# Performance work log

Measured on AMD Instinct MI355X. Metric: run time of the kernel, lower is better.

Reference implementation:

```python
import jax, jax.numpy as jnp
import numpy as np

B, L, D = 1, 2048, 2048
H, KV, HD = 32, 8, 64
REP = H // KV  # GQA repeat factor = 4


def _rope(t, cos, sin):
    # t: (B, L, nH, HD); cos/sin: (L, HD//2). Complex rotation on (even, odd) pairs.
    tr = t.reshape(*t.shape[:-1], HD // 2, 2)
    xr, xi = tr[..., 0], tr[..., 1]
    c = cos[None, :, None, :]
    s = sin[None, :, None, :]
    out_r = xr * c - xi * s
    out_i = xr * s + xi * c
    return jnp.stack([out_r, out_i], axis=-1).reshape(t.shape)


def setup_inputs() -> dict:
    key = jax.random.key(0)
    ks = jax.random.split(key, 5)
    x = jax.random.normal(ks[0], (B, L, D), jnp.float32)
    wq = jax.random.normal(ks[1], (D, H * HD), jnp.float32) * 0.02
    wk = jax.random.normal(ks[2], (D, KV * HD), jnp.float32) * 0.02
    wv = jax.random.normal(ks[3], (D, KV * HD), jnp.float32) * 0.02
    wo = jax.random.normal(ks[4], (H * HD, D), jnp.float32) * 0.02
    pos = jnp.arange(L, dtype=jnp.float32)
    inv_freq = 1.0 / (10000.0 ** (jnp.arange(0, HD, 2, dtype=jnp.float32) / HD))
    ang = pos[:, None] * inv_freq[None, :]  # (L, HD//2)
    freqs_cos = jnp.cos(ang)
    freqs_sin = jnp.sin(ang)
    # causal additive mask (L, L): 0 on/below diagonal, large negative above
    causal = jnp.arange(L)[None, :] <= jnp.arange(L)[:, None]
    mask = jnp.where(causal, 0.0, -1e9).astype(jnp.float32)
    return {"x": x, "wq": wq, "wk": wk, "wv": wv, "wo": wo,
            "freqs_cos": freqs_cos, "freqs_sin": freqs_sin, "mask": mask}


def reference(x, wq, wk, wv, wo, freqs_cos, freqs_sin, mask):
    q = (x @ wq).reshape(B, L, H, HD)
    k = (x @ wk).reshape(B, L, KV, HD)
    v = (x @ wv).reshape(B, L, KV, HD)
    q = _rope(q, freqs_cos, freqs_sin)
    k = _rope(k, freqs_cos, freqs_sin)
    # GQA: repeat_interleave kv heads
    k = jnp.repeat(k, REP, axis=2)
    v = jnp.repeat(v, REP, axis=2)
    # (B, nH, L, HD)
    q = q.transpose(0, 2, 1, 3)
    k = k.transpose(0, 2, 1, 3)
    v = v.transpose(0, 2, 1, 3)
    scores = jnp.einsum('bhqd,bhkd->bhqk', q, k) / np.float32(np.sqrt(HD))
    scores = scores + mask[None, None, :, :]
    attn = jax.nn.softmax(scores.astype(jnp.float32), axis=-1).astype(q.dtype)
    out = jnp.einsum('bhqk,bhkd->bqhd', attn, v).reshape(B, L, H * HD)
    return out @ wo
```

## Files before the change

### kernel.cpp

```cpp
#include <hip/hip_runtime.h>
#include <hip/hip_bf16.h>

#define L 2048
#define D 2048
#define NH 32
#define NKV 8
#define HD 64

typedef unsigned short u16;
typedef __attribute__((ext_vector_type(8))) short bf16x8;
typedef __attribute__((ext_vector_type(4))) float f32x4;

#define QSCALE 0.1803368801f

#define PANEL_OFF(d0, k) ((((size_t)((d0) >> 7) * 64 + ((k) >> 5)) << 12) + (((d0) & 127) << 5) + ((k) & 31))

__device__ __forceinline__ u16 f2bf(float x) {
    __hip_bfloat16 b = __float2bfloat16(x);
    return *reinterpret_cast<u16*>(&b);
}

__device__ __forceinline__ void gload_lds16(const void* g, void* l) {
    __builtin_amdgcn_global_load_lds(
        (const __attribute__((address_space(1))) unsigned int*)g,
        (__attribute__((address_space(3))) unsigned int*)l, 16, 0, 0);
}

__global__ __launch_bounds__(256) void prep_kernel(
    const float* __restrict__ x, u16* __restrict__ xb,
    const float* __restrict__ wq, const float* __restrict__ wk,
    const float* __restrict__ wv, const float* __restrict__ wo,
    u16* __restrict__ wqkvT, u16* __restrict__ woT)
{
    const int z = blockIdx.z;
    if (z == 4) {
        int i = (blockIdx.y * 64 + blockIdx.x) * 256 + threadIdx.x;
        int e = i * 4;
        int row = e >> 11, k0 = e & 2047;
        float4 v = ((const float4*)x)[i];
        ushort4 o;
        o.x = f2bf(v.x); o.y = f2bf(v.y); o.z = f2bf(v.z); o.w = f2bf(v.w);
        *(ushort4*)&xb[PANEL_OFF(row, k0)] = o;
        return;
    }
    const float* src; u16* dst; int C;
    if (z == 0)      { src = wq; dst = wqkvT;                           C = 2048; }
    else if (z == 1) { src = wk; dst = wqkvT + (size_t)2048 * 2048;     C = 512;  }
    else if (z == 2) { src = wv; dst = wqkvT + (size_t)2560 * 2048;     C = 512;  }
    else             { src = wo; dst = woT;                             C = 2048; }
    const int c0 = blockIdx.x * 32;
    if (c0 >= C) return;
    const int r0 = blockIdx.y * 32;
    __shared__ float tile[32][33];
    const int tx = threadIdx.x & 31, ty = threadIdx.x >> 5;
#pragma unroll
    for (int i = 0; i < 32; i += 8)
        tile[ty + i][tx] = src[(size_t)(r0 + ty + i) * C + c0 + tx];
    __syncthreads();
#pragma unroll
    for (int i = 0; i < 32; i += 8) {
        const int n = c0 + ty + i, k = r0 + tx;
        dst[PANEL_OFF(n, k)] = f2bf(tile[tx][ty + i]);
    }
}

#define VT_LDS 72

template <int MODE>
__global__ __launch_bounds__(256) void gemm4w_kernel(
    const u16* __restrict__ A, const u16* __restrict__ Bt, void* __restrict__ Cout,
    int N, int K, const float* __restrict__ fc, const float* __restrict__ fs,
    u16* __restrict__ vt)
{
    __shared__ __align__(16) u16 As[4][128 * 32];
    __shared__ __align__(16) u16 Bs[4][128 * 32];
    const int tid = threadIdx.x;
    const int w = tid >> 6, lane = tid & 63;

    const int nwg = (int)(gridDim.x * gridDim.y);
    int bid = (int)blockIdx.y * (int)gridDim.x + (int)blockIdx.x;
    bid = (bid & 7) * (nwg >> 3) + (bid >> 3);
    const int m0 = (bid / (int)gridDim.x) * 128, n0 = (bid % (int)gridDim.x) * 128;

    const int l15 = lane & 15, quad = lane >> 4, q8 = quad * 8;
    const int wr = (w >> 1) * 64, wc = (w & 1) * 64;
    const int l8 = lane * 8;
    const int wch = w * 1024;

    const u16* pa = A  + ((size_t)(m0 >> 7) * (K / 32) << 12);
    const u16* pb = Bt + ((size_t)(n0 >> 7) * (K / 32) << 12);

    f32x4 acc[4][4];
#pragma unroll
    for (int i = 0; i < 4; ++i)
#pragma unroll
        for (int j = 0; j < 4; ++j) acc[i][j] = (f32x4){0.f, 0.f, 0.f, 0.f};

    const int nSub = K / 32;
    const int nOut = nSub / 2;
#pragma unroll
    for (int s = 0; s < 4; ++s) {
        const size_t so = (size_t)s << 12;
        gload_lds16(pa + so + wch + l8,       &As[s][wch]);
        gload_lds16(pa + so + wch + 512 + l8, &As[s][wch + 512]);
        gload_lds16(pb + so + wch + l8,       &Bs[s][wch]);
        gload_lds16(pb + so + wch + 512 + l8, &Bs[s][wch + 512]);
    }
    for (int it = 0; it < nOut; ++it) {
        const int s0 = 2 * it, cb0 = s0 & 3, cb1 = (s0 + 1) & 3;
        asm volatile("s_waitcnt vmcnt(8)" ::: "memory");
        asm volatile("s_barrier" ::: "memory");
        bf16x8 a0[4], a1[4], b0[4], b1[4];
#pragma unroll
        for (int t = 0; t < 4; ++t) {
            a0[t] = *(const bf16x8*)&As[cb0][(wr + t * 16 + l15) * 32 + q8];
            b0[t] = *(const bf16x8*)&Bs[cb0][(wc + t * 16 + l15) * 32 + q8];
            a1[t] = *(const bf16x8*)&As[cb1][(wr + t * 16 + l15) * 32 + q8];
            b1[t] = *(const bf16x8*)&Bs[cb1][(wc + t * 16 + l15) * 32 + q8];
        }
        asm volatile("s_waitcnt lgkmcnt(0)" ::: "memory");
        asm volatile("s_barrier" ::: "memory");
        {
            const int sp0 = s0 + 4, sp1 = s0 + 5;
            const size_t k0 = (size_t)((sp0 < nSub) ? sp0 : 0) << 12;
            const size_t k1 = (size_t)((sp1 < nSub) ? sp1 : 0) << 12;
            gload_lds16(pa + k0 + wch + l8,       &As[cb0][wch]);
            gload_lds16(pa + k0 + wch + 512 + l8, &As[cb0][wch + 512]);
            gload_lds16(pb + k0 + wch + l8,       &Bs[cb0][wch]);
            gload_lds16(pb + k0 + wch + 512 + l8, &Bs[cb0][wch + 512]);
            gload_lds16(pa + k1 + wch + l8,       &As[cb1][wch]);
            gload_lds16(pa + k1 + wch + 512 + l8, &As[cb1][wch + 512]);
            gload_lds16(pb + k1 + wch + l8,       &Bs[cb1][wch]);
            gload_lds16(pb + k1 + wch + 512 + l8, &Bs[cb1][wch + 512]);
        }
#pragma unroll
        for (int i = 0; i < 4; ++i)
#pragma unroll
            for (int j = 0; j < 4; ++j) {
                acc[i][j] = __builtin_amdgcn_mfma_f32_16x16x32_bf16(a0[i], b0[j], acc[i][j], 0, 0, 0);
                acc[i][j] = __builtin_amdgcn_mfma_f32_16x16x32_bf16(a1[i], b1[j], acc[i][j], 0, 0, 0);
            }
    }

    if (MODE == 0) {
        float* C = (float*)Cout;
#pragma unroll
        for (int i = 0; i < 4; ++i)
#pragma unroll
            for (int j = 0; j < 4; ++j)
#pragma unroll
                for (int r = 0; r < 4; ++r)
                    C[(size_t)(m0 + wr + i * 16 + quad * 4 + r) * N + n0 + wc + j * 16 + l15] = acc[i][j][r];
    } else {
        __syncthreads();
        u16* O = (u16*)Cout;
        const int vc0 = n0 + wc;
        if (vc0 < 2560) {
            const float scl = (vc0 < 2048) ? QSCALE : 1.0f;
            const int odd = l15 & 1;
#pragma unroll
            for (int i = 0; i < 4; ++i)
#pragma unroll
                for (int j = 0; j < 4; ++j)
#pragma unroll
                    for (int r = 0; r < 4; ++r) {
                        const int row = m0 + wr + i * 16 + quad * 4 + r;
                        const int col = vc0 + j * 16 + l15;
                        float v = acc[i][j][r];
                        const int i2 = (j * 16 + l15) >> 1;
                        const float c = fc[row * 32 + i2], s = fs[row * 32 + i2];
                        const float p = __shfl_xor(v, 1);
                        float o = (odd ? (p * s + v * c) : (v * c - p * s)) * scl;
                        O[(size_t)row * 3072 + col] = f2bf(o);
                    }
        } else {
            u16* ws_ = (w < 2 ? (u16*)As : (u16*)Bs) + (w & 1) * (64 * VT_LDS);
#pragma unroll
            for (int i = 0; i < 4; ++i)
#pragma unroll
                for (int j = 0; j < 4; ++j)
#pragma unroll
                    for (int r = 0; r < 4; ++r)
                        ws_[(j * 16 + l15) * VT_LDS + i * 16 + quad * 4 + r] = f2bf(acc[i][j][r]);
#pragma unroll
            for (int t = 0; t < 8; ++t) {
                const int vr = t * 8 + (lane >> 3);
                const int c8 = (lane & 7) * 8;
                bf16x8 vv = *(const bf16x8*)&ws_[vr * VT_LDS + c8];
                *(bf16x8*)&vt[(size_t)(vc0 - 2560 + vr) * 2048 + m0 + wr + c8] = vv;
            }
        }
    }
}

#define ATT_LDK 72
#define ATT_LDP 72

__global__ __launch_bounds__(256) void attn_mfma_kernel(
    const u16* __restrict__ qkv,
    const u16* __restrict__ vt,
    u16* __restrict__ ab)
{
    __shared__ __align__(16) u16 Ks[64 * ATT_LDK];
    __shared__ __align__(16) u16 Vs[64 * ATT_LDK];
    __shared__ __align__(16) u16 Ps[4][16 * ATT_LDP];

    const int h = blockIdx.x;
    const int tile = (int)gridDim.y - 1 - (int)blockIdx.y;
    const int gkv = h >> 2;
    const int tid = threadIdx.x;
    const int w = tid >> 6, lane = tid & 63;
    const int l15 = lane & 15, quad = lane >> 4;
    const int q0 = tile * 64 + w * 16;

    bf16x8 ones;
#pragma unroll
    for (int j = 0; j < 8; ++j) ones[j] = (short)0x3F80;

    bf16x8 qa[2];
    {
        const u16* qrow = qkv + (size_t)(q0 + l15) * 3072 + h * HD + quad * 8;
        qa[0] = *(const bf16x8*)(qrow);
        qa[1] = *(const bf16x8*)(qrow + 32);
    }
    f32x4 O[4];
#pragma unroll
    for (int i = 0; i < 4; ++i) O[i] = (f32x4){0.f, 0.f, 0.f, 0.f};
    float m_run[4], l_run[4];
#pragma unroll
    for (int r = 0; r < 4; ++r) { m_run[r] = -1e30f; l_run[r] = 0.f; }

    for (int c = 0; c <= tile; ++c) {
        const int key0 = c * 64;
        __syncthreads();
#pragma unroll
        for (int i = 0; i < 2; ++i) {
            int slot = tid + 256 * i;
            int r = slot >> 3, o8 = (slot & 7) * 8;
            *(uint4*)&Ks[r * ATT_LDK + o8] =
                *(const uint4*)&qkv[(size_t)(key0 + r) * 3072 + 2048 + gkv * HD + o8];
            *(uint4*)&Vs[r * ATT_LDK + o8] =
                *(const uint4*)&vt[(size_t)(gkv * HD + r) * 2048 + key0 + o8];
        }
        __syncthreads();

        f32x4 S[4];
#pragma unroll
        for (int kt = 0; kt < 4; ++kt) {
            bf16x8 b0 = *(const bf16x8*)&Ks[(kt * 16 + l15) * ATT_LDK + quad * 8];
            bf16x8 b1 = *(const bf16x8*)&Ks[(kt * 16 + l15) * ATT_LDK + 32 + quad * 8];
            f32x4 s = (f32x4){0.f, 0.f, 0.f, 0.f};
            s = __builtin_amdgcn_mfma_f32_16x16x32_bf16(qa[0], b0, s, 0, 0, 0);
            s = __builtin_amdgcn_mfma_f32_16x16x32_bf16(qa[1], b1, s, 0, 0, 0);
            S[kt] = s;
        }
        if (c == tile) {
#pragma unroll
            for (int kt = 0; kt < 4; ++kt) {
                int keyl = kt * 16 + l15;
#pragma unroll
                for (int r = 0; r < 4; ++r)
                    if (keyl > w * 16 + quad * 4 + r) S[kt][r] = -1e30f;
            }
        }
        float alpha[4];
#pragma unroll
        for (int r = 0; r < 4; ++r) {
            float mx = fmaxf(fmaxf(S[0][r], S[1][r]), fmaxf(S[2][r], S[3][r]));
#pragma unroll
            for (int off = 1; off < 16; off <<= 1) mx = fmaxf(mx, __shfl_xor(mx, off));
            float mn = fmaxf(m_run[r], mx);
            alpha[r] = exp2f(m_run[r] - mn);
            m_run[r] = mn;
#pragma unroll
            for (int kt = 0; kt < 4; ++kt) S[kt][r] = exp2f(S[kt][r] - mn);
        }
        u16* pw = Ps[w];
#pragma unroll
        for (int kt = 0; kt < 4; ++kt)
#pragma unroll
            for (int r = 0; r < 4; ++r)
                pw[(quad * 4 + r) * ATT_LDP + kt * 16 + l15] = f2bf(S[kt][r]);
        bf16x8 pa0 = *(const bf16x8*)&pw[l15 * ATT_LDP + quad * 8];
        bf16x8 pa1 = *(const bf16x8*)&pw[l15 * ATT_LDP + 32 + quad * 8];

        f32x4 rs = (f32x4){0.f, 0.f, 0.f, 0.f};
        rs = __builtin_amdgcn_mfma_f32_16x16x32_bf16(pa0, ones, rs, 0, 0, 0);
        rs = __builtin_amdgcn_mfma_f32_16x16x32_bf16(pa1, ones, rs, 0, 0, 0);
#pragma unroll
        for (int r = 0; r < 4; ++r) l_run[r] = l_run[r] * alpha[r] + rs[r];

#pragma unroll
        for (int dt = 0; dt < 4; ++dt)
#pragma unroll
            for (int r = 0; r < 4; ++r) O[dt][r] *= alpha[r];
#pragma unroll
        for (int dt = 0; dt < 4; ++dt) {
            bf16x8 b0 = *(const bf16x8*)&Vs[(dt * 16 + l15) * ATT_LDK + quad * 8];
            bf16x8 b1 = *(const bf16x8*)&Vs[(dt * 16 + l15) * ATT_LDK + 32 + quad * 8];
            O[dt] = __builtin_amdgcn_mfma_f32_16x16x32_bf16(pa0, b0, O[dt], 0, 0, 0);
            O[dt] = __builtin_amdgcn_mfma_f32_16x16x32_bf16(pa1, b1, O[dt], 0, 0, 0);
        }
    }
#pragma unroll
    for (int r = 0; r < 4; ++r) {
        float inv = 1.0f / l_run[r];
        const int q = q0 + quad * 4 + r;
#pragma unroll
        for (int dt = 0; dt < 4; ++dt) {
            const int col = h * HD + dt * 16 + l15;
            ab[PANEL_OFF(q, col)] = f2bf(O[dt][r] * inv);
        }
    }
}

extern "C" void kernel_launch(void* const* d_in, const int* in_sizes, int n_in,
                              void* d_out, int out_size, void* d_ws, size_t ws_size,
                              hipStream_t stream)
{
    const float* x  = (const float*)d_in[0];
    const float* wq = (const float*)d_in[1];
    const float* wk = (const float*)d_in[2];
    const float* wv = (const float*)d_in[3];
    const float* wo = (const float*)d_in[4];
    const float* fc = (const float*)d_in[5];
    const float* fs = (const float*)d_in[6];
    float* out = (float*)d_out;

    u16* xb     = (u16*)d_ws;
    u16* wqkvT  = xb     + (size_t)2048 * 2048;
    u16* woT    = wqkvT  + (size_t)3072 * 2048;
    u16* qkv_bf = woT    + (size_t)2048 * 2048;
    u16* vt     = qkv_bf + (size_t)2048 * 3072;
    u16* ab     = vt     + (size_t)512 * 2048;

    prep_kernel<<<dim3(64, 64, 5), 256, 0, stream>>>(x, xb, wq, wk, wv, wo, wqkvT, woT);

    gemm4w_kernel<1><<<dim3(3072 / 128, 2048 / 128), 256, 0, stream>>>(
        xb, wqkvT, qkv_bf, 3072, 2048, fc, fs, vt);

    attn_mfma_kernel<<<dim3(NH, L / 64), 256, 0, stream>>>(qkv_bf, vt, ab);

    gemm4w_kernel<0><<<dim3(2048 / 128, 2048 / 128), 256, 0, stream>>>(
        ab, woT, out, 2048, 2048, nullptr, nullptr, nullptr);
}
```

Baseline: 278.0 us.

## Double-buffer attention K/V tiles via async global-to-LDS loads with XOR swizzle

Replaces the synchronous register-staged K/V tile loads in the attention kernel with direct global-to-LDS loads into two ping-pong buffers, prefetching the next key chunk while the current one is consumed. Padded LDS rows are replaced by an XOR swizzle to avoid bank conflicts, and MFMA sections get raised wave priority. This aims to hide global load latency and cut barriers per iteration. It costs more LDS, and correctness depends on hand-written waitcnt and barrier placement.

New measurement: 249.8 us. 10.1% less time.

```diff
diff --git a/kernel.cpp b/kernel.cpp
--- a/kernel.cpp
+++ b/kernel.cpp
@@ -193,7 +193,6 @@
     }
 }
 
-#define ATT_LDK 72
 #define ATT_LDP 72
 
 __global__ __launch_bounds__(256) void attn_mfma_kernel(
@@ -201,8 +200,8 @@
     const u16* __restrict__ vt,
     u16* __restrict__ ab)
 {
-    __shared__ __align__(16) u16 Ks[64 * ATT_LDK];
-    __shared__ __align__(16) u16 Vs[64 * ATT_LDK];
+    __shared__ __align__(16) u16 Ks[2][64 * 64];
+    __shared__ __align__(16) u16 Vs[2][64 * 64];
     __shared__ __align__(16) u16 Ps[4][16 * ATT_LDP];
 
     const int h = blockIdx.x;
@@ -213,6 +212,12 @@
     const int l15 = lane & 15, quad = lane >> 4;
     const int q0 = tile * 64 + w * 16;
 
+    const int srow = lane >> 3, schunk = lane & 7;
+    const int r0_ = w * 16 + srow, r1_ = w * 16 + 8 + srow;
+    const int c0_ = (schunk ^ (r0_ & 7)) * 8, c1_ = (schunk ^ (r1_ & 7)) * 8;
+    const u16* kbase = qkv + 2048 + gkv * HD;
+    const u16* vbase = vt + (size_t)gkv * HD * 2048;
+
     bf16x8 ones;
 #pragma unroll
     for (int j = 0; j < 8; ++j) ones[j] = (short)0x3F80;
@@ -230,30 +235,34 @@
 #pragma unroll
     for (int r = 0; r < 4; ++r) { m_run[r] = -1e30f; l_run[r] = 0.f; }
 
+    gload_lds16(kbase + (size_t)r0_ * 3072 + c0_,        &Ks[0][(w * 16) * 64]);
+    gload_lds16(kbase + (size_t)r1_ * 3072 + c1_,        &Ks[0][(w * 16 + 8) * 64]);
+    gload_lds16(vbase + (size_t)r0_ * 2048 + c0_,        &Vs[0][(w * 16) * 64]);
+    gload_lds16(vbase + (size_t)r1_ * 2048 + c1_,        &Vs[0][(w * 16 + 8) * 64]);
+
     for (int c = 0; c <= tile; ++c) {
-        const int key0 = c * 64;
-        __syncthreads();
-#pragma unroll
-        for (int i = 0; i < 2; ++i) {
-            int slot = tid + 256 * i;
-            int r = slot >> 3, o8 = (slot & 7) * 8;
-            *(uint4*)&Ks[r * ATT_LDK + o8] =
-                *(const uint4*)&qkv[(size_t)(key0 + r) * 3072 + 2048 + gkv * HD + o8];
-            *(uint4*)&Vs[r * ATT_LDK + o8] =
-                *(const uint4*)&vt[(size_t)(gkv * HD + r) * 2048 + key0 + o8];
-        }
-        __syncthreads();
+        const int cb = c & 1, nb = cb ^ 1;
+        const int kn = (c < tile ? c + 1 : tile) * 64;
+        gload_lds16(kbase + (size_t)(kn + r0_) * 3072 + c0_, &Ks[nb][(w * 16) * 64]);
+        gload_lds16(kbase + (size_t)(kn + r1_) * 3072 + c1_, &Ks[nb][(w * 16 + 8) * 64]);
+        gload_lds16(vbase + (size_t)r0_ * 2048 + kn + c0_,   &Vs[nb][(w * 16) * 64]);
+        gload_lds16(vbase + (size_t)r1_ * 2048 + kn + c1_,   &Vs[nb][(w * 16 + 8) * 64]);
+        asm volatile("s_waitcnt vmcnt(4)" ::: "memory");
+        asm volatile("s_barrier" ::: "memory");
 
         f32x4 S[4];
+        __builtin_amdgcn_s_setprio(1);
 #pragma unroll
         for (int kt = 0; kt < 4; ++kt) {
-            bf16x8 b0 = *(const bf16x8*)&Ks[(kt * 16 + l15) * ATT_LDK + quad * 8];
-            bf16x8 b1 = *(const bf16x8*)&Ks[(kt * 16 + l15) * ATT_LDK + 32 + quad * 8];
+            const int kr = kt * 16 + l15, kx = (kr & 7);
+            bf16x8 b0 = *(const bf16x8*)&Ks[cb][kr * 64 + ((quad ^ kx) * 8)];
+            bf16x8 b1 = *(const bf16x8*)&Ks[cb][kr * 64 + (((quad + 4) ^ kx) * 8)];
             f32x4 s = (f32x4){0.f, 0.f, 0.f, 0.f};
             s = __builtin_amdgcn_mfma_f32_16x16x32_bf16(qa[0], b0, s, 0, 0, 0);
             s = __builtin_amdgcn_mfma_f32_16x16x32_bf16(qa[1], b1, s, 0, 0, 0);
             S[kt] = s;
         }
+        __builtin_amdgcn_s_setprio(0);
         if (c == tile) {
 #pragma unroll
             for (int kt = 0; kt < 4; ++kt) {
@@ -294,22 +303,27 @@
         for (int dt = 0; dt < 4; ++dt)
 #pragma unroll
             for (int r = 0; r < 4; ++r) O[dt][r] *= alpha[r];
+        __builtin_amdgcn_s_setprio(1);
 #pragma unroll
         for (int dt = 0; dt < 4; ++dt) {
-            bf16x8 b0 = *(const bf16x8*)&Vs[(dt * 16 + l15) * ATT_LDK + quad * 8];
-            bf16x8 b1 = *(const bf16x8*)&Vs[(dt * 16 + l15) * ATT_LDK + 32 + quad * 8];
+            const int vr = dt * 16 + l15, vx = (vr & 7);
+            bf16x8 b0 = *(const bf16x8*)&Vs[cb][vr * 64 + ((quad ^ vx) * 8)];
+            bf16x8 b1 = *(const bf16x8*)&Vs[cb][vr * 64 + (((quad + 4) ^ vx) * 8)];
             O[dt] = __builtin_amdgcn_mfma_f32_16x16x32_bf16(pa0, b0, O[dt], 0, 0, 0);
             O[dt] = __builtin_amdgcn_mfma_f32_16x16x32_bf16(pa1, b1, O[dt], 0, 0, 0);
         }
+        __builtin_amdgcn_s_setprio(0);
+        asm volatile("s_barrier" ::: "memory");
     }
 #pragma unroll
     for (int r = 0; r < 4; ++r) {
         float inv = 1.0f / l_run[r];
         const int q = q0 + quad * 4 + r;
+        const int pbase = ((q >> 7) << 18) + ((q & 127) << 5);
 #pragma unroll
         for (int dt = 0; dt < 4; ++dt) {
             const int col = h * HD + dt * 16 + l15;
-            ab[PANEL_OFF(q, col)] = f2bf(O[dt][r] * inv);
+            ab[pbase + ((col >> 5) << 12) + (col & 31)] = f2bf(O[dt][r] * inv);
         }
     }
 }
```
